# Kernel tuning notes

Hardware: AMD Instinct MI355X
Metric: run time of the kernel (lower is better)

Reference implementation:

```python
import jax, jax.numpy as jnp
import numpy as np

# Grid / model dims
B, H, W = 1, 90, 180
P = H * W                 # 16200 spatial points
MODEL_DIM = 130
L = MODEL_DIM - 2         # learnable_dim = 128
NH, HD = 8, 16            # n_heads, head_dim
S = 16                    # shared_hidden (DISCO out_channels)
K = 25                    # number of DISCO basis functions (piecewise-linear 5x5)
NNB = 25                  # neighbors per output point (theta_cutoff stencil)
MH = 32                   # head MLP hidden
FH = 256                  # FFN hidden


def setup_inputs() -> dict:
    key = jax.random.key(0)
    ks = jax.random.split(key, 12)
    x = jax.random.normal(ks[0], (B, H, W, MODEL_DIM), dtype=jnp.float32)
    # sparse DISCO structure: neighbor indices + precomputed (quadrature-weighted) basis values
    nbr_idx = jax.random.randint(ks[1], (P, NNB), 0, P, dtype=jnp.int32)
    basis_vals = jax.random.normal(ks[2], (K, P, NNB), dtype=jnp.float32) * 0.1
    # learnable DISCO kernel weights (out_channels=S, in_channels=1, K basis coeffs) + bias
    disco_w = jax.random.normal(ks[3], (S, K), dtype=jnp.float32) / np.sqrt(K).astype(np.float32)
    disco_b = jax.random.normal(ks[4], (S,), dtype=jnp.float32) * 0.01
    # per-head MLP params: S -> MH -> 1, one set per head
    head_w1 = jax.random.normal(ks[5], (NH, S, MH), dtype=jnp.float32) / np.sqrt(S).astype(np.float32)
    head_b1 = jnp.zeros((NH, MH), dtype=jnp.float32)
    head_w2 = jax.random.normal(ks[6], (NH, MH, 1), dtype=jnp.float32) / np.sqrt(MH).astype(np.float32)
    head_b2 = jnp.zeros((NH, 1), dtype=jnp.float32)
    # FFN: model_dim -> FH -> L, with the sin/cos input columns zeroed (as in __init__)
    ffn_w1 = jax.random.normal(ks[7], (MODEL_DIM, FH), dtype=jnp.float32) / np.sqrt(MODEL_DIM).astype(np.float32)
    ffn_w1 = ffn_w1.at[-2:, :].set(0.0)
    ffn_b1 = jnp.zeros((FH,), dtype=jnp.float32)
    ffn_w2 = jax.random.normal(ks[8], (FH, L), dtype=jnp.float32) / np.sqrt(FH).astype(np.float32)
    ffn_b2 = jnp.zeros((L,), dtype=jnp.float32)
    return dict(x=x, nbr_idx=nbr_idx, basis_vals=basis_vals, disco_w=disco_w, disco_b=disco_b,
                head_w1=head_w1, head_b1=head_b1, head_w2=head_w2, head_b2=head_b2,
                ffn_w1=ffn_w1, ffn_b1=ffn_b1, ffn_w2=ffn_w2, ffn_b2=ffn_b2)


def reference(x, nbr_idx, basis_vals, disco_w, disco_b,
              head_w1, head_b1, head_w2, head_b2,
              ffn_w1, ffn_b1, ffn_w2, ffn_b2):
    gelu = lambda t: jax.nn.gelu(t, approximate=False)  # torch nn.GELU default is exact
    x_learn = x[..., :L]          # (B,H,W,L)
    sin_cos = x[..., L:]          # (B,H,W,2)
    x_res = x_learn

    # ---- DISCO spherical conv, depthwise over B*L channels (in_channels=1) ----
    xf = jnp.transpose(x_learn, (0, 3, 1, 2)).reshape(B * L, P)      # (N, P)
    gathered = xf[:, nbr_idx]                                        # (N, P, NNB) irregular gather
    z = jnp.einsum('kpn,cpn->ckp', basis_vals, gathered)             # (N, K, P) basis projections
    y = jnp.einsum('sk,ckp->csp', disco_w, z) + disco_b[None, :, None]  # (N, S, P)
    disco_out = y.reshape(B, L, S, H, W).transpose(0, 3, 4, 1, 2)    # (B,H,W,L,S)

    # ---- per-head MLP, vectorized over heads ----
    hfeat = disco_out.reshape(B, H, W, NH, HD, S)                    # (B,H,W,NH,HD,S)
    h1 = gelu(jnp.einsum('bxyhds,hsm->bxyhdm', hfeat, head_w1) + head_b1[:, None, :])
    hout = jnp.einsum('bxyhdm,hmo->bxyhdo', h1, head_w2) + head_b2[:, None, :]  # o=1
    x_mix = hout.reshape(B, H, W, L)                                 # heads concatenated in order
    x_mix = x_mix + x_res                                            # residual

    # ---- FFN channel mixing on [x_mix, sin_cos] ----
    x_full = jnp.concatenate([x_mix, sin_cos], axis=-1)              # (B,H,W,MODEL_DIM)
    hf = gelu(jnp.einsum('bxyd,df->bxyf', x_full, ffn_w1) + ffn_b1)
    x_ffn = jnp.einsum('bxyf,fl->bxyl', hf, ffn_w2) + ffn_b2
    x_out = x_ffn + x_mix
    return jnp.concatenate([x_out, sin_cos], axis=-1)                # (B,H,W,MODEL_DIM)
```

## Files before the change

kernel.cpp:

```cpp
#include <hip/hip_runtime.h>
#include <hip/hip_bf16.h>

#define P_TOT 16200
#define MODEL_DIMC 130
#define L_DIM 128
#define NHH 8
#define S_DIM 16
#define K_DIM 25
#define NNBC 25
#define MH_DIM 32
#define FH_DIM 256

__device__ __forceinline__ float gelu_f(float x) {
    float z = fabsf(x) * 0.70710678118654752440f;
    float t = __builtin_amdgcn_rcpf(fmaf(0.3275911f, z, 1.0f));
    float poly = t * fmaf(t, fmaf(t, fmaf(t, fmaf(t, 1.061405429f, -1.453152027f),
                                          1.421413741f), -0.284496736f), 0.254829592f);
    float e = __expf(-z * z);
    float erfp = fmaf(-poly, e, 1.0f);
    float erfv = copysignf(erfp, x);
    return 0.5f * x * (1.0f + erfv);
}

__global__ __launch_bounds__(256) void k0_transpose_w1(const float* __restrict__ hw1,
                                                       float* __restrict__ w1t) {
    int i = blockIdx.x * 256 + threadIdx.x;
    if (i < NHH * S_DIM * MH_DIM) {
        int h = i >> 9, s = (i >> 5) & 15, m = i & 31;
        w1t[h * 512 + m * 16 + s] = hw1[i];
    }
}

__global__ __launch_bounds__(256) void k1_bw(const float* __restrict__ basis,
                                             const float* __restrict__ disco_w,
                                             float* __restrict__ bw) {
    __shared__ float w[S_DIM * K_DIM];
    int tid = threadIdx.x;
    for (int i = tid; i < S_DIM * K_DIM; i += 256) w[i] = disco_w[i];
    __syncthreads();
    int i = blockIdx.x * 256 + tid;
    if (i >= P_TOT * NNBC) return;
    float bv[K_DIM];
#pragma unroll
    for (int k = 0; k < K_DIM; k++) bv[k] = basis[k * (P_TOT * NNBC) + i];
    float acc[S_DIM];
#pragma unroll
    for (int s = 0; s < S_DIM; s++) {
        float a = 0.f;
#pragma unroll
        for (int k = 0; k < K_DIM; k++) a = fmaf(w[s * K_DIM + k], bv[k], a);
        acc[s] = a;
    }
    float4* outp = (float4*)(bw + (size_t)i * S_DIM);
#pragma unroll
    for (int q = 0; q < 4; q++) {
        float4 v; v.x = acc[q*4+0]; v.y = acc[q*4+1]; v.z = acc[q*4+2]; v.w = acc[q*4+3];
        outp[q] = v;
    }
}

#define YSTR 2056
__global__ __launch_bounds__(256, 4) void k2_disco_head(
        const float* __restrict__ x, const int* __restrict__ nbr,
        const float* __restrict__ bw, const float* __restrict__ w1t,
        const float* __restrict__ head_b1, const float* __restrict__ head_w2,
        const float* __restrict__ head_b2, const float* __restrict__ disco_b,
        float* __restrict__ xmix) {
    __shared__ float ylds[4 * YSTR];

    int tid  = threadIdx.x;
    int lane = tid & 63;
    int wv   = __builtin_amdgcn_readfirstlane(tid >> 6);
    int p0   = blockIdx.x * 4;
    int p    = p0 + wv;

    const float* bwp = bw + (size_t)p * (NNBC * S_DIM);
    const int*   nbp = nbr + p * NNBC;

    float y0[16], y1[16];
#pragma unroll
    for (int s = 0; s < 16; s++) { float db = disco_b[s]; y0[s] = db; y1[s] = db; }

    const float* xb0 = x + lane;
    const float* xb1 = x + 64 + lane;

#pragma unroll 1
    for (int nb = 0; nb < 24; nb += 4) {
#pragma unroll
        for (int j = 0; j < 4; j++) {
            int u = nbp[nb + j];
            float g0 = xb0[(size_t)u * MODEL_DIMC];
            float g1 = xb1[(size_t)u * MODEL_DIMC];
#pragma unroll
            for (int s = 0; s < 16; s++) {
                float wv_ = bwp[(nb + j) * 16 + s];
                y0[s] = fmaf(g0, wv_, y0[s]);
                y1[s] = fmaf(g1, wv_, y1[s]);
            }
        }
    }
    {
        int u = nbp[24];
        float g0 = xb0[(size_t)u * MODEL_DIMC];
        float g1 = xb1[(size_t)u * MODEL_DIMC];
#pragma unroll
        for (int s = 0; s < 16; s++) {
            float wv_ = bwp[24 * 16 + s];
            y0[s] = fmaf(g0, wv_, y0[s]);
            y1[s] = fmaf(g1, wv_, y1[s]);
        }
    }

#pragma unroll
    for (int s = 0; s < 16; s++) {
        ylds[wv * YSTR + s * 128 + lane]      = y0[s];
        ylds[wv * YSTR + s * 128 + 64 + lane] = y1[s];
    }
    __syncthreads();

    int ptl = lane >> 4;
    int d   = lane & 15;
#pragma unroll
    for (int t = 0; t < 2; t++) {
        int hh = __builtin_amdgcn_readfirstlane(wv + 4 * t);
        float yv[16];
#pragma unroll
        for (int s = 0; s < 16; s++)
            yv[s] = ylds[ptl * YSTR + s * 128 + hh * 16 + d];
        const float* wrow = w1t + hh * (MH_DIM * S_DIM);
        const float* b1r  = head_b1 + hh * MH_DIM;
        const float* w2r  = head_w2 + hh * MH_DIM;
        float acc = head_b2[hh];
#pragma unroll 2
        for (int m = 0; m < MH_DIM; m++) {
            float a = b1r[m];
#pragma unroll
            for (int s = 0; s < 16; s++)
                a = fmaf(yv[s], wrow[m * 16 + s], a);
            a = gelu_f(a);
            acc = fmaf(a, w2r[m], acc);
        }
        int pp = p0 + ptl;
        int c  = hh * 16 + d;
        xmix[pp * L_DIM + c] = acc + x[(size_t)pp * MODEL_DIMC + c];
    }
}

__global__ __launch_bounds__(256, 4) void k3a_ffn1(
        const float* __restrict__ xmix, const float* __restrict__ w1,
        const float* __restrict__ b1, float* __restrict__ hf) {
    __shared__ __align__(16) float xm[32 * 132];
    int tid = threadIdx.x;
    int p0 = blockIdx.x * 32;
    int valid = min(32, P_TOT - p0);
    {
        const float4* src = (const float4*)(xmix + (size_t)p0 * L_DIM);
        for (int j = tid; j < valid * 32; j += 256) {
            float4 v = src[j];
            int pt = j >> 5, q = j & 31;
            *(float4*)&xm[pt * 132 + q * 4] = v;
        }
    }
    __syncthreads();

    int fg = tid & 15, pg = tid >> 4;
    int f0 = fg * 16;
    float acc[2][16];
#pragma unroll
    for (int j = 0; j < 16; j++) { float bb = b1[f0 + j]; acc[0][j] = bb; acc[1][j] = bb; }
    const float* xr0 = &xm[(pg * 2 + 0) * 132];
    const float* xr1 = &xm[(pg * 2 + 1) * 132];
#pragma unroll 2
    for (int k = 0; k < 128; k++) {
        float xa = xr0[k], xb = xr1[k];
        const float4* wr = (const float4*)&w1[k * FH_DIM + f0];
#pragma unroll
        for (int q = 0; q < 4; q++) {
            float4 w4 = wr[q];
            acc[0][q*4+0] = fmaf(xa, w4.x, acc[0][q*4+0]);
            acc[0][q*4+1] = fmaf(xa, w4.y, acc[0][q*4+1]);
            acc[0][q*4+2] = fmaf(xa, w4.z, acc[0][q*4+2]);
            acc[0][q*4+3] = fmaf(xa, w4.w, acc[0][q*4+3]);
            acc[1][q*4+0] = fmaf(xb, w4.x, acc[1][q*4+0]);
            acc[1][q*4+1] = fmaf(xb, w4.y, acc[1][q*4+1]);
            acc[1][q*4+2] = fmaf(xb, w4.z, acc[1][q*4+2]);
            acc[1][q*4+3] = fmaf(xb, w4.w, acc[1][q*4+3]);
        }
    }
#pragma unroll
    for (int i = 0; i < 2; i++) {
        int pl = pg * 2 + i;
        if (pl < valid) {
            float4* hp = (float4*)(hf + (size_t)(p0 + pl) * FH_DIM + f0);
#pragma unroll
            for (int q = 0; q < 4; q++) {
                float4 v;
                v.x = gelu_f(acc[i][q*4+0]);
                v.y = gelu_f(acc[i][q*4+1]);
                v.z = gelu_f(acc[i][q*4+2]);
                v.w = gelu_f(acc[i][q*4+3]);
                hp[q] = v;
            }
        }
    }
}

__global__ __launch_bounds__(256, 4) void k3b_ffn2(
        const float* __restrict__ x, const float* __restrict__ xmix,
        const float* __restrict__ hf, const float* __restrict__ w2,
        const float* __restrict__ b2, float* __restrict__ out) {
    __shared__ __align__(16) float hfl[32 * 260];
    int tid = threadIdx.x;
    int p0 = blockIdx.x * 32;
    int valid = min(32, P_TOT - p0);
    {
        const float4* src = (const float4*)(hf + (size_t)p0 * FH_DIM);
        for (int j = tid; j < valid * 64; j += 256) {
            float4 v = src[j];
            int pt = j >> 6, q = j & 63;
            *(float4*)&hfl[pt * 260 + q * 4] = v;
        }
    }
    __syncthreads();

    int lg = tid & 31, pg = tid >> 5;
    float4 bb = *(const float4*)&b2[lg * 4];
    float acc2[4][4];
#pragma unroll
    for (int i = 0; i < 4; i++) {
        acc2[i][0] = bb.x; acc2[i][1] = bb.y; acc2[i][2] = bb.z; acc2[i][3] = bb.w;
    }
#pragma unroll 2
    for (int f = 0; f < FH_DIM; f++) {
        float4 wv4 = *(const float4*)&w2[f * L_DIM + lg * 4];
#pragma unroll
        for (int i = 0; i < 4; i++) {
            float hv = hfl[(pg * 4 + i) * 260 + f];
            acc2[i][0] = fmaf(hv, wv4.x, acc2[i][0]);
            acc2[i][1] = fmaf(hv, wv4.y, acc2[i][1]);
            acc2[i][2] = fmaf(hv, wv4.z, acc2[i][2]);
            acc2[i][3] = fmaf(hv, wv4.w, acc2[i][3]);
        }
    }
#pragma unroll
    for (int i = 0; i < 4; i++) {
        int pl = pg * 4 + i;
        if (pl < valid) {
            int pp = p0 + pl;
            float4 xm4 = *(const float4*)&xmix[(size_t)pp * L_DIM + lg * 4];
            float2 o01, o23;
            o01.x = acc2[i][0] + xm4.x;
            o01.y = acc2[i][1] + xm4.y;
            o23.x = acc2[i][2] + xm4.z;
            o23.y = acc2[i][3] + xm4.w;
            *(float2*)&out[(size_t)pp * MODEL_DIMC + lg * 4]     = o01;
            *(float2*)&out[(size_t)pp * MODEL_DIMC + lg * 4 + 2] = o23;
        }
    }
    if (tid < 64) {
        int pt = tid >> 1, wch = tid & 1;
        if (pt < valid) {
            int pp = p0 + pt;
            out[(size_t)pp * MODEL_DIMC + 128 + wch] = x[(size_t)pp * MODEL_DIMC + 128 + wch];
        }
    }
}

extern "C" void kernel_launch(void* const* d_in, const int* in_sizes, int n_in,
                              void* d_out, int out_size, void* d_ws, size_t ws_size,
                              hipStream_t stream) {
    const float* x        = (const float*)d_in[0];
    const int*   nbr      = (const int*)  d_in[1];
    const float* basis    = (const float*)d_in[2];
    const float* disco_w  = (const float*)d_in[3];
    const float* disco_b  = (const float*)d_in[4];
    const float* head_w1  = (const float*)d_in[5];
    const float* head_b1  = (const float*)d_in[6];
    const float* head_w2  = (const float*)d_in[7];
    const float* head_b2  = (const float*)d_in[8];
    const float* ffn_w1   = (const float*)d_in[9];
    const float* ffn_b1   = (const float*)d_in[10];
    const float* ffn_w2   = (const float*)d_in[11];
    const float* ffn_b2   = (const float*)d_in[12];
    float* out = (float*)d_out;

    float* bw   = (float*)d_ws;
    float* xmix = bw + (size_t)P_TOT * NNBC * S_DIM;
    float* w1t  = xmix + (size_t)P_TOT * L_DIM;
    float* hf   = bw;

    hipLaunchKernelGGL(k0_transpose_w1, dim3(16), dim3(256), 0, stream, head_w1, w1t);
    hipLaunchKernelGGL(k1_bw, dim3((P_TOT * NNBC + 255) / 256), dim3(256), 0, stream,
                       basis, disco_w, bw);
    hipLaunchKernelGGL(k2_disco_head, dim3(P_TOT / 4), dim3(256), 0, stream,
                       x, nbr, bw, w1t, head_b1, head_w2, head_b2, disco_b, xmix);
    hipLaunchKernelGGL(k3a_ffn1, dim3((P_TOT + 31) / 32), dim3(256), 0, stream,
                       xmix, ffn_w1, ffn_b1, hf);
    hipLaunchKernelGGL(k3b_ffn2, dim3((P_TOT + 31) / 32), dim3(256), 0, stream,
                       x, xmix, hf, ffn_w2, ffn_b2, out);
}
```

Before: 323.0 us.

## Retile FFN GEMMs with vectorized k-blocking and preload DISCO neighbor indices

Both FFN kernels now handle 16 points per block instead of 32. Each thread computes a 4x4 (ffn1) or 2x4 (ffn2) output tile over 4-wide k-chunks, reading float4 from shared memory and four float4 weight rows per step. The DISCO gather kernel preloads all 25 neighbor indices into registers and processes two neighbors per iteration so more independent gathers are in flight. Launch bounds drop from 4 to 2 waves per SIMD, which gives more registers per thread but may lower occupancy. Halving the point tile doubles the number of global weight reads per point in the FFN kernels.

```diff
diff --git a/kernel.cpp b/kernel.cpp
--- a/kernel.cpp
+++ b/kernel.cpp
@@ -60,7 +60,7 @@
 }
 
 #define YSTR 2056
-__global__ __launch_bounds__(256, 4) void k2_disco_head(
+__global__ __launch_bounds__(256, 2) void k2_disco_head(
         const float* __restrict__ x, const int* __restrict__ nbr,
         const float* __restrict__ bw, const float* __restrict__ w1t,
         const float* __restrict__ head_b1, const float* __restrict__ head_w2,
@@ -77,6 +77,10 @@
     const float* bwp = bw + (size_t)p * (NNBC * S_DIM);
     const int*   nbp = nbr + p * NNBC;
 
+    int un[NNBC];
+#pragma unroll
+    for (int j = 0; j < NNBC; j++) un[j] = nbp[j];
+
     float y0[16], y1[16];
 #pragma unroll
     for (int s = 0; s < 16; s++) { float db = disco_b[s]; y0[s] = db; y1[s] = db; }
@@ -85,22 +89,24 @@
     const float* xb1 = x + 64 + lane;
 
 #pragma unroll 1
-    for (int nb = 0; nb < 24; nb += 4) {
-#pragma unroll
-        for (int j = 0; j < 4; j++) {
-            int u = nbp[nb + j];
-            float g0 = xb0[(size_t)u * MODEL_DIMC];
-            float g1 = xb1[(size_t)u * MODEL_DIMC];
-#pragma unroll
-            for (int s = 0; s < 16; s++) {
-                float wv_ = bwp[(nb + j) * 16 + s];
-                y0[s] = fmaf(g0, wv_, y0[s]);
-                y1[s] = fmaf(g1, wv_, y1[s]);
-            }
+    for (int nb = 0; nb < 24; nb += 2) {
+        int u0 = un[nb], u1 = un[nb + 1];
+        float g00 = xb0[(size_t)u0 * MODEL_DIMC];
+        float g01 = xb1[(size_t)u0 * MODEL_DIMC];
+        float g10 = xb0[(size_t)u1 * MODEL_DIMC];
+        float g11 = xb1[(size_t)u1 * MODEL_DIMC];
+#pragma unroll
+        for (int s = 0; s < 16; s++) {
+            float w0 = bwp[nb * 16 + s];
+            float w1_ = bwp[nb * 16 + 16 + s];
+            y0[s] = fmaf(g00, w0, y0[s]);
+            y1[s] = fmaf(g01, w0, y1[s]);
+            y0[s] = fmaf(g10, w1_, y0[s]);
+            y1[s] = fmaf(g11, w1_, y1[s]);
         }
     }
     {
-        int u = nbp[24];
+        int u = un[24];
         float g0 = xb0[(size_t)u * MODEL_DIMC];
         float g1 = xb1[(size_t)u * MODEL_DIMC];
 #pragma unroll
@@ -146,13 +152,13 @@
     }
 }
 
-__global__ __launch_bounds__(256, 4) void k3a_ffn1(
+__global__ __launch_bounds__(256, 2) void k3a_ffn1(
         const float* __restrict__ xmix, const float* __restrict__ w1,
         const float* __restrict__ b1, float* __restrict__ hf) {
-    __shared__ __align__(16) float xm[32 * 132];
+    __shared__ __align__(16) float xm[16 * 132];
     int tid = threadIdx.x;
-    int p0 = blockIdx.x * 32;
-    int valid = min(32, P_TOT - p0);
+    int p0 = blockIdx.x * 16;
+    int valid = min(16, P_TOT - p0);
     {
         const float4* src = (const float4*)(xmix + (size_t)p0 * L_DIM);
         for (int j = tid; j < valid * 32; j += 256) {
@@ -163,101 +169,124 @@
     }
     __syncthreads();
 
-    int fg = tid & 15, pg = tid >> 4;
-    int f0 = fg * 16;
-    float acc[2][16];
-#pragma unroll
-    for (int j = 0; j < 16; j++) { float bb = b1[f0 + j]; acc[0][j] = bb; acc[1][j] = bb; }
-    const float* xr0 = &xm[(pg * 2 + 0) * 132];
-    const float* xr1 = &xm[(pg * 2 + 1) * 132];
+    int fid = tid & 63, pid = tid >> 6;
+    int f0 = fid * 4;
+    float4 bb = *(const float4*)&b1[f0];
+    float acc[4][4];
+#pragma unroll
+    for (int i = 0; i < 4; i++) {
+        acc[i][0] = bb.x; acc[i][1] = bb.y; acc[i][2] = bb.z; acc[i][3] = bb.w;
+    }
 #pragma unroll 2
-    for (int k = 0; k < 128; k++) {
-        float xa = xr0[k], xb = xr1[k];
-        const float4* wr = (const float4*)&w1[k * FH_DIM + f0];
-#pragma unroll
-        for (int q = 0; q < 4; q++) {
-            float4 w4 = wr[q];
-            acc[0][q*4+0] = fmaf(xa, w4.x, acc[0][q*4+0]);
-            acc[0][q*4+1] = fmaf(xa, w4.y, acc[0][q*4+1]);
-            acc[0][q*4+2] = fmaf(xa, w4.z, acc[0][q*4+2]);
-            acc[0][q*4+3] = fmaf(xa, w4.w, acc[0][q*4+3]);
-            acc[1][q*4+0] = fmaf(xb, w4.x, acc[1][q*4+0]);
-            acc[1][q*4+1] = fmaf(xb, w4.y, acc[1][q*4+1]);
-            acc[1][q*4+2] = fmaf(xb, w4.z, acc[1][q*4+2]);
-            acc[1][q*4+3] = fmaf(xb, w4.w, acc[1][q*4+3]);
-        }
-    }
-#pragma unroll
-    for (int i = 0; i < 2; i++) {
-        int pl = pg * 2 + i;
+    for (int k0 = 0; k0 < 128; k0 += 4) {
+        float4 w4[4];
+#pragma unroll
+        for (int j = 0; j < 4; j++)
+            w4[j] = *(const float4*)&w1[(k0 + j) * FH_DIM + f0];
+#pragma unroll
+        for (int i = 0; i < 4; i++) {
+            float4 xv = *(const float4*)&xm[(pid * 4 + i) * 132 + k0];
+            acc[i][0] = fmaf(xv.x, w4[0].x, acc[i][0]);
+            acc[i][1] = fmaf(xv.x, w4[0].y, acc[i][1]);
+            acc[i][2] = fmaf(xv.x, w4[0].z, acc[i][2]);
+            acc[i][3] = fmaf(xv.x, w4[0].w, acc[i][3]);
+            acc[i][0] = fmaf(xv.y, w4[1].x, acc[i][0]);
+            acc[i][1] = fmaf(xv.y, w4[1].y, acc[i][1]);
+            acc[i][2] = fmaf(xv.y, w4[1].z, acc[i][2]);
+            acc[i][3] = fmaf(xv.y, w4[1].w, acc[i][3]);
+            acc[i][0] = fmaf(xv.z, w4[2].x, acc[i][0]);
+            acc[i][1] = fmaf(xv.z, w4[2].y, acc[i][1]);
+            acc[i][2] = fmaf(xv.z, w4[2].z, acc[i][2]);
+            acc[i][3] = fmaf(xv.z, w4[2].w, acc[i][3]);
+            acc[i][0] = fmaf(xv.w, w4[3].x, acc[i][0]);
+            acc[i][1] = fmaf(xv.w, w4[3].y, acc[i][1]);
+            acc[i][2] = fmaf(xv.w, w4[3].z, acc[i][2]);
+            acc[i][3] = fmaf(xv.w, w4[3].w, acc[i][3]);
+        }
+    }
+#pragma unroll
+    for (int i = 0; i < 4; i++) {
+        int pl = pid * 4 + i;
         if (pl < valid) {
-            float4* hp = (float4*)(hf + (size_t)(p0 + pl) * FH_DIM + f0);
-#pragma unroll
-            for (int q = 0; q < 4; q++) {
-                float4 v;
-                v.x = gelu_f(acc[i][q*4+0]);
-                v.y = gelu_f(acc[i][q*4+1]);
-                v.z = gelu_f(acc[i][q*4+2]);
-                v.w = gelu_f(acc[i][q*4+3]);
-                hp[q] = v;
-            }
-        }
-    }
-}
-
-__global__ __launch_bounds__(256, 4) void k3b_ffn2(
+            float4 v;
+            v.x = gelu_f(acc[i][0]);
+            v.y = gelu_f(acc[i][1]);
+            v.z = gelu_f(acc[i][2]);
+            v.w = gelu_f(acc[i][3]);
+            *(float4*)&hf[(size_t)(p0 + pl) * FH_DIM + f0] = v;
+        }
+    }
+}
+
+__global__ __launch_bounds__(256, 2) void k3b_ffn2(
         const float* __restrict__ x, const float* __restrict__ xmix,
         const float* __restrict__ hf, const float* __restrict__ w2,
         const float* __restrict__ b2, float* __restrict__ out) {
-    __shared__ __align__(16) float hfl[32 * 260];
+    __shared__ __align__(16) float hfl[16 * 264];
     int tid = threadIdx.x;
-    int p0 = blockIdx.x * 32;
-    int valid = min(32, P_TOT - p0);
+    int p0 = blockIdx.x * 16;
+    int valid = min(16, P_TOT - p0);
     {
         const float4* src = (const float4*)(hf + (size_t)p0 * FH_DIM);
         for (int j = tid; j < valid * 64; j += 256) {
             float4 v = src[j];
             int pt = j >> 6, q = j & 63;
-            *(float4*)&hfl[pt * 260 + q * 4] = v;
+            *(float4*)&hfl[pt * 264 + q * 4] = v;
         }
     }
     __syncthreads();
 
-    int lg = tid & 31, pg = tid >> 5;
-    float4 bb = *(const float4*)&b2[lg * 4];
-    float acc2[4][4];
-#pragma unroll
-    for (int i = 0; i < 4; i++) {
-        acc2[i][0] = bb.x; acc2[i][1] = bb.y; acc2[i][2] = bb.z; acc2[i][3] = bb.w;
+    int lid = tid & 31, pid = tid >> 5;
+    int l0 = lid * 4;
+    float4 bb = *(const float4*)&b2[l0];
+    float acc[2][4];
+#pragma unroll
+    for (int i = 0; i < 2; i++) {
+        acc[i][0] = bb.x; acc[i][1] = bb.y; acc[i][2] = bb.z; acc[i][3] = bb.w;
     }
 #pragma unroll 2
-    for (int f = 0; f < FH_DIM; f++) {
-        float4 wv4 = *(const float4*)&w2[f * L_DIM + lg * 4];
-#pragma unroll
-        for (int i = 0; i < 4; i++) {
-            float hv = hfl[(pg * 4 + i) * 260 + f];
-            acc2[i][0] = fmaf(hv, wv4.x, acc2[i][0]);
-            acc2[i][1] = fmaf(hv, wv4.y, acc2[i][1]);
-            acc2[i][2] = fmaf(hv, wv4.z, acc2[i][2]);
-            acc2[i][3] = fmaf(hv, wv4.w, acc2[i][3]);
-        }
-    }
-#pragma unroll
-    for (int i = 0; i < 4; i++) {
-        int pl = pg * 4 + i;
+    for (int f0 = 0; f0 < FH_DIM; f0 += 4) {
+        float4 w4[4];
+#pragma unroll
+        for (int j = 0; j < 4; j++)
+            w4[j] = *(const float4*)&w2[(f0 + j) * L_DIM + l0];
+#pragma unroll
+        for (int i = 0; i < 2; i++) {
+            float4 hv = *(const float4*)&hfl[(pid * 2 + i) * 264 + f0];
+            acc[i][0] = fmaf(hv.x, w4[0].x, acc[i][0]);
+            acc[i][1] = fmaf(hv.x, w4[0].y, acc[i][1]);
+            acc[i][2] = fmaf(hv.x, w4[0].z, acc[i][2]);
+            acc[i][3] = fmaf(hv.x, w4[0].w, acc[i][3]);
+            acc[i][0] = fmaf(hv.y, w4[1].x, acc[i][0]);
+            acc[i][1] = fmaf(hv.y, w4[1].y, acc[i][1]);
+            acc[i][2] = fmaf(hv.y, w4[1].z, acc[i][2]);
+            acc[i][3] = fmaf(hv.y, w4[1].w, acc[i][3]);
+            acc[i][0] = fmaf(hv.z, w4[2].x, acc[i][0]);
+            acc[i][1] = fmaf(hv.z, w4[2].y, acc[i][1]);
+            acc[i][2] = fmaf(hv.z, w4[2].z, acc[i][2]);
+            acc[i][3] = fmaf(hv.z, w4[2].w, acc[i][3]);
+            acc[i][0] = fmaf(hv.w, w4[3].x, acc[i][0]);
+            acc[i][1] = fmaf(hv.w, w4[3].y, acc[i][1]);
+            acc[i][2] = fmaf(hv.w, w4[3].z, acc[i][2]);
+            acc[i][3] = fmaf(hv.w, w4[3].w, acc[i][3]);
+        }
+    }
+#pragma unroll
+    for (int i = 0; i < 2; i++) {
+        int pl = pid * 2 + i;
         if (pl < valid) {
             int pp = p0 + pl;
-            float4 xm4 = *(const float4*)&xmix[(size_t)pp * L_DIM + lg * 4];
+            float4 xm4 = *(const float4*)&xmix[(size_t)pp * L_DIM + l0];
             float2 o01, o23;
-            o01.x = acc2[i][0] + xm4.x;
-            o01.y = acc2[i][1] + xm4.y;
-            o23.x = acc2[i][2] + xm4.z;
-            o23.y = acc2[i][3] + xm4.w;
-            *(float2*)&out[(size_t)pp * MODEL_DIMC + lg * 4]     = o01;
-            *(float2*)&out[(size_t)pp * MODEL_DIMC + lg * 4 + 2] = o23;
-        }
-    }
-    if (tid < 64) {
+            o01.x = acc[i][0] + xm4.x;
+            o01.y = acc[i][1] + xm4.y;
+            o23.x = acc[i][2] + xm4.z;
+            o23.y = acc[i][3] + xm4.w;
+            *(float2*)&out[(size_t)pp * MODEL_DIMC + l0]     = o01;
+            *(float2*)&out[(size_t)pp * MODEL_DIMC + l0 + 2] = o23;
+        }
+    }
+    if (tid < 32) {
         int pt = tid >> 1, wch = tid & 1;
         if (pt < valid) {
             int pp = p0 + pt;
@@ -294,8 +323,8 @@
                        basis, disco_w, bw);
     hipLaunchKernelGGL(k2_disco_head, dim3(P_TOT / 4), dim3(256), 0, stream,
                        x, nbr, bw, w1t, head_b1, head_w2, head_b2, disco_b, xmix);
-    hipLaunchKernelGGL(k3a_ffn1, dim3((P_TOT + 31) / 32), dim3(256), 0, stream,
+    hipLaunchKernelGGL(k3a_ffn1, dim3((P_TOT + 15) / 16), dim3(256), 0, stream,
                        xmix, ffn_w1, ffn_b1, hf);
-    hipLaunchKernelGGL(k3b_ffn2, dim3((P_TOT + 31) / 32), dim3(256), 0, stream,
+    hipLaunchKernelGGL(k3b_ffn2, dim3((P_TOT + 15) / 16), dim3(256), 0, stream,
                        x, xmix, hf, ffn_w2, ffn_b2, out);
 }
```

Measured after the change: 272.8 us. 1.18x faster.
